# Kernel tuning notes

Hardware: AMD Instinct MI355X
Metric: run time of the kernel (lower is better)

Reference implementation:

```python
import jax, jax.numpy as jnp
import numpy as np

N_NODES = 100000
N_EDGES = 1600000
IN_C = 256
H1 = 128
H2 = 64
OUT_C = 64


def setup_inputs() -> dict:
    key = jax.random.key(0)
    ks = jax.random.split(key, 8)
    x = jax.random.normal(ks[0], (N_NODES, IN_C), dtype=jnp.float32)
    edge_src = jax.random.randint(ks[1], (N_EDGES,), 0, N_NODES, dtype=jnp.int32)
    edge_dst = jax.random.randint(ks[2], (N_EDGES,), 0, N_NODES, dtype=jnp.int32)
    edge_weight = jax.random.uniform(ks[3], (N_EDGES,), dtype=jnp.float32)
    W1 = jax.random.normal(ks[4], (IN_C, H1), dtype=jnp.float32) / np.sqrt(IN_C)
    b1 = jnp.zeros((H1,), dtype=jnp.float32)
    W2 = jax.random.normal(ks[5], (H1, H2), dtype=jnp.float32) / np.sqrt(H1)
    b2 = jnp.zeros((H2,), dtype=jnp.float32)
    W3 = jax.random.normal(ks[6], (H2, OUT_C), dtype=jnp.float32) / np.sqrt(H2)
    b3 = jnp.zeros((OUT_C,), dtype=jnp.float32)
    return dict(x=x, edge_src=edge_src, edge_dst=edge_dst, edge_weight=edge_weight,
                W1=W1, b1=b1, W2=W2, b2=b2, W3=W3, b3=b3)


def _gcn_layer(h, W, b, src, dst, ew):
    # GraphConvolution: out = adj @ (h @ W) + b, adj given as weighted edge list
    support = h @ W                      # [N, d_out] dense GEMM
    msg = support[src] * ew[:, None]     # [E, d_out] gather (irregular access)
    agg = jax.ops.segment_sum(msg, dst, num_segments=N_NODES)  # SpMM scatter-add
    return agg + b


def reference(x, edge_src, edge_dst, edge_weight, W1, b1, W2, b2, W3, b3):
    # Eval-mode forward: dropout is identity (training=False)
    h = jax.nn.relu(_gcn_layer(x, W1, b1, edge_src, edge_dst, edge_weight))
    h = jax.nn.relu(_gcn_layer(h, W2, b2, edge_src, edge_dst, edge_weight))
    out = _gcn_layer(h, W3, b3, edge_src, edge_dst, edge_weight)
    return out
```

## Files before the change

### kernel.cpp

```cpp
#include <hip/hip_runtime.h>
#include <hip/hip_bf16.h>


#define EPB 8192

__device__ __forceinline__ unsigned short f2bf(float f) {
    unsigned int u = __float_as_uint(f);
    unsigned int r = (u + 0x7fffu + ((u >> 16) & 1u)) >> 16;
    return (unsigned short)r;
}

using frag_ab = __attribute__((ext_vector_type(8))) short;
using frag_cd = __attribute__((ext_vector_type(4))) float;

template <int BN>
__global__ __launch_bounds__(256) void mfma_gemm_kernel(
    const float* __restrict__ A, const unsigned short* __restrict__ WT,
    unsigned short* __restrict__ C, int M, int K)
{
    constexpr int BM = 64, BK = 64;
    constexpr int LDA = BK + 8;
    __shared__ unsigned short As[BM * LDA];
    __shared__ unsigned short Bs[BN * LDA];

    const int tid = threadIdx.x;
    const int wave = tid >> 6;
    const int lane = tid & 63;
    const int quad = lane >> 4;
    const int l16 = lane & 15;
    const int m0 = blockIdx.x * BM;

    frag_cd acc[BN / 16];
#pragma unroll
    for (int f = 0; f < BN / 16; ++f) acc[f] = (frag_cd){0.f, 0.f, 0.f, 0.f};

    for (int k0 = 0; k0 < K; k0 += BK) {
#pragma unroll
        for (int i = 0; i < 4; ++i) {
            const int linear = (i * 256 + tid) * 4;
            const int r = linear >> 6;
            const int c = linear & 63;
            const int row = m0 + r;
            float4 v = make_float4(0.f, 0.f, 0.f, 0.f);
            if (row < M) v = *(const float4*)&A[(size_t)row * K + k0 + c];
            ushort4 u;
            u.x = f2bf(v.x); u.y = f2bf(v.y); u.z = f2bf(v.z); u.w = f2bf(v.w);
            *(ushort4*)&As[r * LDA + c] = u;
        }
#pragma unroll
        for (int i = 0; i < BN / 32; ++i) {
            const int linear = (i * 256 + tid) * 8;
            const int n = linear >> 6;
            const int c = linear & 63;
            const uint4 u = *(const uint4*)&WT[(size_t)n * K + k0 + c];
            *(uint4*)&Bs[n * LDA + c] = u;
        }
        __syncthreads();

#pragma unroll
        for (int ks = 0; ks < 2; ++ks) {
            const int kk = ks * 32 + quad * 8;
            const frag_ab a = *(const frag_ab*)&As[(wave * 16 + l16) * LDA + kk];
#pragma unroll
            for (int f = 0; f < BN / 16; ++f) {
                const frag_ab b = *(const frag_ab*)&Bs[(f * 16 + l16) * LDA + kk];
                acc[f] = __builtin_amdgcn_mfma_f32_16x16x32_bf16(a, b, acc[f], 0, 0, 0);
            }
        }
        __syncthreads();
    }

#pragma unroll
    for (int f = 0; f < BN / 16; ++f) {
#pragma unroll
        for (int r = 0; r < 4; ++r) {
            const int row = m0 + wave * 16 + quad * 4 + r;
            if (row < M) C[(size_t)row * BN + f * 16 + l16] = f2bf(acc[f][r]);
        }
    }
}

__global__ __launch_bounds__(256) void wt_kernel(
    const float* __restrict__ W1, const float* __restrict__ W2, const float* __restrict__ W3,
    unsigned short* __restrict__ WT1, unsigned short* __restrict__ WT2, unsigned short* __restrict__ WT3)
{
    const int i = blockIdx.x * 256 + threadIdx.x;
    const float* W; unsigned short* WT; int K, N, j;
    if (i < 32768)      { W = W1; WT = WT1; K = 256; N = 128; j = i; }
    else if (i < 40960) { W = W2; WT = WT2; K = 128; N = 64;  j = i - 32768; }
    else if (i < 45056) { W = W3; WT = WT3; K = 64;  N = 64;  j = i - 40960; }
    else return;
    const int n = j / K, k = j % K;
    WT[j] = f2bf(W[k * N + n]);
}

__global__ __launch_bounds__(256) void zero_int_kernel(int* __restrict__ p, int n)
{
    const int i = blockIdx.x * 256 + threadIdx.x;
    if (i < n) p[i] = 0;
}

__global__ __launch_bounds__(256) void hist_kernel(
    const int* __restrict__ dst, int* __restrict__ deg, int E)
{
    const int e = blockIdx.x * 256 + threadIdx.x;
    if (e < E) atomicAdd(&deg[dst[e]], 1);
}

__global__ __launch_bounds__(256) void scan1_kernel(
    const int* __restrict__ deg, int* __restrict__ offs, int* __restrict__ bsum, int n)
{
    __shared__ int tmp[256];
    const int i = blockIdx.x * 256 + threadIdx.x;
    const int v = (i < n) ? deg[i] : 0;
    tmp[threadIdx.x] = v;
    __syncthreads();
#pragma unroll
    for (int d = 1; d < 256; d <<= 1) {
        const int t = (threadIdx.x >= d) ? tmp[threadIdx.x - d] : 0;
        __syncthreads();
        tmp[threadIdx.x] += t;
        __syncthreads();
    }
    if (i < n) offs[i] = tmp[threadIdx.x] - v;
    if (threadIdx.x == 255) bsum[blockIdx.x] = tmp[255];
}

__global__ __launch_bounds__(512) void scan2_kernel(int* __restrict__ bsum, int nb)
{
    __shared__ int tmp[512];
    const int v = ((int)threadIdx.x < nb) ? bsum[threadIdx.x] : 0;
    tmp[threadIdx.x] = v;
    __syncthreads();
#pragma unroll
    for (int d = 1; d < 512; d <<= 1) {
        const int t = ((int)threadIdx.x >= d) ? tmp[threadIdx.x - d] : 0;
        __syncthreads();
        tmp[threadIdx.x] += t;
        __syncthreads();
    }
    if ((int)threadIdx.x < nb) bsum[threadIdx.x] = tmp[threadIdx.x] - v;
}

__global__ __launch_bounds__(256) void scan3_kernel(
    int* __restrict__ offs, const int* __restrict__ bsum, int n, int E)
{
    const int i = blockIdx.x * 256 + threadIdx.x;
    if (i < n) offs[i] += bsum[blockIdx.x];
    if (i == 0) offs[n] = E;
}

__global__ __launch_bounds__(256) void count_kernel(
    const int* __restrict__ dst, int* __restrict__ cmat, int E, int nblk, int nbuck)
{
    __shared__ int hist[1600];
    for (int i = threadIdx.x; i < nbuck; i += 256) hist[i] = 0;
    __syncthreads();
    const int base = blockIdx.x * EPB;
    const int end = min(base + EPB, E);
    for (int e = base + threadIdx.x; e < end; e += 256)
        atomicAdd(&hist[dst[e] >> 6], 1);
    __syncthreads();
    for (int i = threadIdx.x; i < nbuck; i += 256)
        cmat[(size_t)i * nblk + blockIdx.x] = hist[i];
}

__global__ __launch_bounds__(256) void scanA_kernel(
    int* __restrict__ data, int* __restrict__ psum, int L)
{
    __shared__ int tmp[256];
    const int b0 = blockIdx.x * 1024 + threadIdx.x * 4;
    int v[4] = {0, 0, 0, 0};
    if (b0 + 3 < L) { const int4 t = *(const int4*)&data[b0]; v[0]=t.x; v[1]=t.y; v[2]=t.z; v[3]=t.w; }
    else { for (int i = 0; i < 4; ++i) if (b0 + i < L) v[i] = data[b0 + i]; }
    const int s = v[0] + v[1] + v[2] + v[3];
    tmp[threadIdx.x] = s;
    __syncthreads();
#pragma unroll
    for (int d = 1; d < 256; d <<= 1) {
        const int t = (threadIdx.x >= d) ? tmp[threadIdx.x - d] : 0;
        __syncthreads();
        tmp[threadIdx.x] += t;
        __syncthreads();
    }
    int run = tmp[threadIdx.x] - s;
    int o[4];
#pragma unroll
    for (int i = 0; i < 4; ++i) { o[i] = run; run += v[i]; }
    if (b0 + 3 < L) { *(int4*)&data[b0] = make_int4(o[0], o[1], o[2], o[3]); }
    else { for (int i = 0; i < 4; ++i) if (b0 + i < L) data[b0 + i] = o[i]; }
    if (threadIdx.x == 255) psum[blockIdx.x] = tmp[255];
}

__global__ __launch_bounds__(1024) void scanB_kernel(int* __restrict__ psum, int nb)
{
    __shared__ int tmp[1024];
    const int v = ((int)threadIdx.x < nb) ? psum[threadIdx.x] : 0;
    tmp[threadIdx.x] = v;
    __syncthreads();
#pragma unroll
    for (int d = 1; d < 1024; d <<= 1) {
        const int t = ((int)threadIdx.x >= d) ? tmp[threadIdx.x - d] : 0;
        __syncthreads();
        tmp[threadIdx.x] += t;
        __syncthreads();
    }
    if ((int)threadIdx.x < nb) psum[threadIdx.x] = tmp[threadIdx.x] - v;
}

__global__ __launch_bounds__(256) void scanC_kernel(
    int* __restrict__ data, const int* __restrict__ psum, int L)
{
    const int i = blockIdx.x * 256 + threadIdx.x;
    if (i < L) data[i] += psum[i >> 10];
}

__global__ __launch_bounds__(256) void place_kernel(
    const int* __restrict__ src, const int* __restrict__ dst, const float* __restrict__ ew,
    const int* __restrict__ cmat, uint2* __restrict__ ebuck, int E, int nblk, int nbuck)
{
    __shared__ int cursor[1600];
    const int k = blockIdx.x;
    for (int i = threadIdx.x; i < nbuck; i += 256)
        cursor[i] = cmat[(size_t)i * nblk + k];
    __syncthreads();
    const int base = k * EPB;
    const int end = min(base + EPB, E);
    for (int e = base + threadIdx.x; e < end; e += 256) {
        const int d = dst[e];
        const int b = d >> 6;
        const int pos = atomicAdd(&cursor[b], 1);
        ebuck[pos] = make_uint2(((unsigned)src[e] << 6) | (unsigned)(d & 63),
                                __float_as_uint(ew[e]));
    }
}

__global__ __launch_bounds__(256) void sort2_kernel(
    const uint2* __restrict__ ebuck, const int* __restrict__ offs,
    uint2* __restrict__ ecsr, int N)
{
    __shared__ int cur[64];
    const int b = blockIdx.x;
    const int node0 = b << 6;
    const int nn = min(64, N - node0);
    if ((int)threadIdx.x < nn) cur[threadIdx.x] = offs[node0 + threadIdx.x];
    __syncthreads();
    const int j0 = offs[node0];
    const int j1 = offs[node0 + nn];
    for (int j = j0 + (int)threadIdx.x; j < j1; j += 256) {
        const uint2 ed = ebuck[j];
        const int dl = (int)(ed.x & 63u);
        const int pos = atomicAdd(&cur[dl], 1);
        ecsr[pos] = make_uint2(ed.x >> 6, ed.y);
    }
}

template <int D, int LOGT, bool RELU>
__global__ __launch_bounds__(256) void gather_agg_kernel(
    const unsigned short* __restrict__ S, const int* __restrict__ offs,
    const uint2* __restrict__ ecsr,
    const float* __restrict__ bias, float* __restrict__ out, int N)
{
    const int TPN = 1 << LOGT;
    const int gid = blockIdx.x * 256 + threadIdx.x;
    const int node = gid >> LOGT;
    if (node >= N) return;
    const int lane = gid & (TPN - 1);
    const int c8 = lane << 3;

    const int j0 = offs[node];
    const int j1 = offs[node + 1];

    float acc[8];
#pragma unroll
    for (int c = 0; c < 8; ++c) acc[c] = 0.f;

    for (int jb = j0; jb < j1; jb += TPN) {
        const int j = jb + lane;
        int myc = 0;
        float myw = 0.f;
        if (j < j1) {
            const uint2 p = ecsr[j];
            myc = (int)p.x;
            myw = __uint_as_float(p.y);
        }
        const int cnt = min(TPN, j1 - jb);
        for (int t = 0; t < cnt; ++t) {
            const int s = __shfl(myc, t, TPN);
            const float w = __shfl(myw, t, TPN);
            const uint4 v = *(const uint4*)&S[(size_t)s * D + c8];
#pragma unroll
            for (int q = 0; q < 4; ++q) {
                const unsigned int u = (&v.x)[q];
                const float lo = __uint_as_float(u << 16);
                const float hi = __uint_as_float(u & 0xffff0000u);
                acc[q * 2 + 0] += w * lo;
                acc[q * 2 + 1] += w * hi;
            }
        }
    }

#pragma unroll
    for (int c = 0; c < 8; ++c) {
        float v = acc[c] + bias[c8 + c];
        if (RELU) v = fmaxf(v, 0.f);
        acc[c] = v;
    }
    float4* op = (float4*)&out[(size_t)node * D + c8];
    op[0] = make_float4(acc[0], acc[1], acc[2], acc[3]);
    op[1] = make_float4(acc[4], acc[5], acc[6], acc[7]);
}

extern "C" void kernel_launch(void* const* d_in, const int* in_sizes, int n_in,
                              void* d_out, int out_size, void* d_ws, size_t ws_size,
                              hipStream_t stream)
{
    const float* x    = (const float*)d_in[0];
    const int*   esrc = (const int*)  d_in[1];
    const int*   edst = (const int*)  d_in[2];
    const float* ew   = (const float*)d_in[3];
    const float* W1   = (const float*)d_in[4];
    const float* b1   = (const float*)d_in[5];
    const float* W2   = (const float*)d_in[6];
    const float* b2   = (const float*)d_in[7];
    const float* W3   = (const float*)d_in[8];
    const float* b3   = (const float*)d_in[9];

    const int N = in_sizes[0] / 256;
    const int E = in_sizes[1];

    const int nbuck = (N + 63) >> 6;
    const int nblk = (E + EPB - 1) / EPB;
    const int L = nbuck * nblk;

    unsigned short* Sb = (unsigned short*)d_ws;
    float* H   = (float*)(Sb + (size_t)N * 128);
    unsigned short* WT1 = (unsigned short*)(H + (size_t)N * 128);
    unsigned short* WT2 = WT1 + 256 * 128;
    unsigned short* WT3 = WT2 + 128 * 64;
    uint2* ebuck = (uint2*)(WT3 + 64 * 64);
    uint2* ecsr  = ebuck + E;
    int* deg    = (int*)(ecsr + E);
    int* offs   = deg + N;
    int* bsum   = offs + N + 4;
    int* cmat   = bsum + 512;
    int* psum   = cmat + ((L + 3) & ~3);
    float* out  = (float*)d_out;

    const dim3 blk(256);
    const int nblkN = (N + 255) / 256;
    const int nblkE = (E + 255) / 256;
    const int mblocks = (N + 63) / 64;

    wt_kernel<<<(45056 + 255) / 256, blk, 0, stream>>>(W1, W2, W3, WT1, WT2, WT3);
    zero_int_kernel<<<nblkN, blk, 0, stream>>>(deg, N);
    hist_kernel<<<nblkE, blk, 0, stream>>>(edst, deg, E);
    scan1_kernel<<<nblkN, blk, 0, stream>>>(deg, offs, bsum, N);
    scan2_kernel<<<1, 512, 0, stream>>>(bsum, nblkN);
    scan3_kernel<<<nblkN, blk, 0, stream>>>(offs, bsum, N, E);
    count_kernel<<<nblk, blk, 0, stream>>>(edst, cmat, E, nblk, nbuck);
    scanA_kernel<<<(L + 1023) / 1024, blk, 0, stream>>>(cmat, psum, L);
    scanB_kernel<<<1, 1024, 0, stream>>>(psum, (L + 1023) / 1024);
    scanC_kernel<<<(L + 255) / 256, blk, 0, stream>>>(cmat, psum, L);
    place_kernel<<<nblk, blk, 0, stream>>>(esrc, edst, ew, cmat, ebuck, E, nblk, nbuck);
    sort2_kernel<<<nbuck, blk, 0, stream>>>(ebuck, offs, ecsr, N);

    mfma_gemm_kernel<128><<<mblocks, blk, 0, stream>>>(x, WT1, Sb, N, 256);
    gather_agg_kernel<128, 4, true><<<((N * 16) + 255) / 256, blk, 0, stream>>>(
        Sb, offs, ecsr, b1, H, N);

    mfma_gemm_kernel<64><<<mblocks, blk, 0, stream>>>(H, WT2, Sb, N, 128);
    gather_agg_kernel<64, 3, true><<<((N * 8) + 255) / 256, blk, 0, stream>>>(
        Sb, offs, ecsr, b2, H, N);

    mfma_gemm_kernel<64><<<mblocks, blk, 0, stream>>>(H, WT3, Sb, N, 64);
    gather_agg_kernel<64, 3, false><<<((N * 8) + 255) / 256, blk, 0, stream>>>(
        Sb, offs, ecsr, b3, out, N);
}
```

Measured before the change: 520.3 us.

## Derive CSR offsets in sort pass, enlarge GEMM row tile, unroll full gather chunks

The separate degree histogram and three-kernel scan are removed. Per-node CSR offsets are now computed inside sort2 from a local 64-bin count and wave prefix scan, with bucket bounds taken from the already-scanned count matrix. This drops five launches and a global atomic pass over all edges. The MFMA GEMM now computes 128 rows per block with two accumulator sets, so each B fragment is reused twice, at the cost of more registers and fewer blocks. The gather loop gains a fully unrolled fast path for full TPN chunks, with a masked tail loop for the remainder.

```diff
diff --git a/kernel.cpp b/kernel.cpp
--- a/kernel.cpp
+++ b/kernel.cpp
@@ -18,7 +18,7 @@
     const float* __restrict__ A, const unsigned short* __restrict__ WT,
     unsigned short* __restrict__ C, int M, int K)
 {
-    constexpr int BM = 64, BK = 64;
+    constexpr int BM = 128, BK = 64;
     constexpr int LDA = BK + 8;
     __shared__ unsigned short As[BM * LDA];
     __shared__ unsigned short Bs[BN * LDA];
@@ -30,13 +30,15 @@
     const int l16 = lane & 15;
     const int m0 = blockIdx.x * BM;
 
-    frag_cd acc[BN / 16];
-#pragma unroll
-    for (int f = 0; f < BN / 16; ++f) acc[f] = (frag_cd){0.f, 0.f, 0.f, 0.f};
+    frag_cd acc[2][BN / 16];
+#pragma unroll
+    for (int rt = 0; rt < 2; ++rt)
+#pragma unroll
+        for (int f = 0; f < BN / 16; ++f) acc[rt][f] = (frag_cd){0.f, 0.f, 0.f, 0.f};
 
     for (int k0 = 0; k0 < K; k0 += BK) {
 #pragma unroll
-        for (int i = 0; i < 4; ++i) {
+        for (int i = 0; i < 8; ++i) {
             const int linear = (i * 256 + tid) * 4;
             const int r = linear >> 6;
             const int c = linear & 63;
@@ -60,24 +62,27 @@
 #pragma unroll
         for (int ks = 0; ks < 2; ++ks) {
             const int kk = ks * 32 + quad * 8;
-            const frag_ab a = *(const frag_ab*)&As[(wave * 16 + l16) * LDA + kk];
+            const frag_ab a0 = *(const frag_ab*)&As[(wave * 32 + l16) * LDA + kk];
+            const frag_ab a1 = *(const frag_ab*)&As[(wave * 32 + 16 + l16) * LDA + kk];
 #pragma unroll
             for (int f = 0; f < BN / 16; ++f) {
                 const frag_ab b = *(const frag_ab*)&Bs[(f * 16 + l16) * LDA + kk];
-                acc[f] = __builtin_amdgcn_mfma_f32_16x16x32_bf16(a, b, acc[f], 0, 0, 0);
+                acc[0][f] = __builtin_amdgcn_mfma_f32_16x16x32_bf16(a0, b, acc[0][f], 0, 0, 0);
+                acc[1][f] = __builtin_amdgcn_mfma_f32_16x16x32_bf16(a1, b, acc[1][f], 0, 0, 0);
             }
         }
         __syncthreads();
     }
 
 #pragma unroll
-    for (int f = 0; f < BN / 16; ++f) {
-#pragma unroll
-        for (int r = 0; r < 4; ++r) {
-            const int row = m0 + wave * 16 + quad * 4 + r;
-            if (row < M) C[(size_t)row * BN + f * 16 + l16] = f2bf(acc[f][r]);
-        }
-    }
+    for (int rt = 0; rt < 2; ++rt)
+#pragma unroll
+        for (int f = 0; f < BN / 16; ++f)
+#pragma unroll
+            for (int r = 0; r < 4; ++r) {
+                const int row = m0 + wave * 32 + rt * 16 + quad * 4 + r;
+                if (row < M) C[(size_t)row * BN + f * 16 + l16] = f2bf(acc[rt][f][r]);
+            }
 }
 
 __global__ __launch_bounds__(256) void wt_kernel(
@@ -94,62 +99,6 @@
     WT[j] = f2bf(W[k * N + n]);
 }
 
-__global__ __launch_bounds__(256) void zero_int_kernel(int* __restrict__ p, int n)
-{
-    const int i = blockIdx.x * 256 + threadIdx.x;
-    if (i < n) p[i] = 0;
-}
-
-__global__ __launch_bounds__(256) void hist_kernel(
-    const int* __restrict__ dst, int* __restrict__ deg, int E)
-{
-    const int e = blockIdx.x * 256 + threadIdx.x;
-    if (e < E) atomicAdd(&deg[dst[e]], 1);
-}
-
-__global__ __launch_bounds__(256) void scan1_kernel(
-    const int* __restrict__ deg, int* __restrict__ offs, int* __restrict__ bsum, int n)
-{
-    __shared__ int tmp[256];
-    const int i = blockIdx.x * 256 + threadIdx.x;
-    const int v = (i < n) ? deg[i] : 0;
-    tmp[threadIdx.x] = v;
-    __syncthreads();
-#pragma unroll
-    for (int d = 1; d < 256; d <<= 1) {
-        const int t = (threadIdx.x >= d) ? tmp[threadIdx.x - d] : 0;
-        __syncthreads();
-        tmp[threadIdx.x] += t;
-        __syncthreads();
-    }
-    if (i < n) offs[i] = tmp[threadIdx.x] - v;
-    if (threadIdx.x == 255) bsum[blockIdx.x] = tmp[255];
-}
-
-__global__ __launch_bounds__(512) void scan2_kernel(int* __restrict__ bsum, int nb)
-{
-    __shared__ int tmp[512];
-    const int v = ((int)threadIdx.x < nb) ? bsum[threadIdx.x] : 0;
-    tmp[threadIdx.x] = v;
-    __syncthreads();
-#pragma unroll
-    for (int d = 1; d < 512; d <<= 1) {
-        const int t = ((int)threadIdx.x >= d) ? tmp[threadIdx.x - d] : 0;
-        __syncthreads();
-        tmp[threadIdx.x] += t;
-        __syncthreads();
-    }
-    if ((int)threadIdx.x < nb) bsum[threadIdx.x] = tmp[threadIdx.x] - v;
-}
-
-__global__ __launch_bounds__(256) void scan3_kernel(
-    int* __restrict__ offs, const int* __restrict__ bsum, int n, int E)
-{
-    const int i = blockIdx.x * 256 + threadIdx.x;
-    if (i < n) offs[i] += bsum[blockIdx.x];
-    if (i == 0) offs[n] = E;
-}
-
 __global__ __launch_bounds__(256) void count_kernel(
     const int* __restrict__ dst, int* __restrict__ cmat, int E, int nblk, int nbuck)
 {
@@ -236,21 +185,42 @@
 }
 
 __global__ __launch_bounds__(256) void sort2_kernel(
-    const uint2* __restrict__ ebuck, const int* __restrict__ offs,
-    uint2* __restrict__ ecsr, int N)
-{
+    const uint2* __restrict__ ebuck, const int* __restrict__ cmat,
+    int* __restrict__ offs, uint2* __restrict__ ecsr,
+    int N, int nblk, int nbuck, int E)
+{
+    __shared__ int cnt[64];
     __shared__ int cur[64];
     const int b = blockIdx.x;
     const int node0 = b << 6;
     const int nn = min(64, N - node0);
-    if ((int)threadIdx.x < nn) cur[threadIdx.x] = offs[node0 + threadIdx.x];
-    __syncthreads();
-    const int j0 = offs[node0];
-    const int j1 = offs[node0 + nn];
+    const int j0 = cmat[(size_t)b * nblk];
+    const int j1 = (b + 1 < nbuck) ? cmat[(size_t)(b + 1) * nblk] : E;
+
+    if (threadIdx.x < 64) cnt[threadIdx.x] = 0;
+    __syncthreads();
+    for (int j = j0 + (int)threadIdx.x; j < j1; j += 256)
+        atomicAdd(&cnt[ebuck[j].x & 63u], 1);
+    __syncthreads();
+
+    if (threadIdx.x < 64) {
+        const int myv = cnt[threadIdx.x];
+        int v = myv;
+#pragma unroll
+        for (int d = 1; d < 64; d <<= 1) {
+            const int t = __shfl_up(v, d, 64);
+            if ((int)threadIdx.x >= d) v += t;
+        }
+        const int base = j0 + v - myv;
+        cur[threadIdx.x] = base;
+        if ((int)threadIdx.x < nn) offs[node0 + threadIdx.x] = base;
+        if (threadIdx.x == 0 && b == nbuck - 1) offs[N] = E;
+    }
+    __syncthreads();
+
     for (int j = j0 + (int)threadIdx.x; j < j1; j += 256) {
         const uint2 ed = ebuck[j];
-        const int dl = (int)(ed.x & 63u);
-        const int pos = atomicAdd(&cur[dl], 1);
+        const int pos = atomicAdd(&cur[ed.x & 63u], 1);
         ecsr[pos] = make_uint2(ed.x >> 6, ed.y);
     }
 }
@@ -275,7 +245,25 @@
 #pragma unroll
     for (int c = 0; c < 8; ++c) acc[c] = 0.f;
 
-    for (int jb = j0; jb < j1; jb += TPN) {
+    int jb = j0;
+    for (; jb + TPN <= j1; jb += TPN) {
+        const uint2 p = ecsr[jb + lane];
+        const int myc = (int)p.x;
+        const float myw = __uint_as_float(p.y);
+#pragma unroll
+        for (int t = 0; t < TPN; ++t) {
+            const int s = __shfl(myc, t, TPN);
+            const float w = __shfl(myw, t, TPN);
+            const uint4 v = *(const uint4*)&S[(size_t)s * D + c8];
+#pragma unroll
+            for (int q = 0; q < 4; ++q) {
+                const unsigned int u = (&v.x)[q];
+                acc[q * 2 + 0] += w * __uint_as_float(u << 16);
+                acc[q * 2 + 1] += w * __uint_as_float(u & 0xffff0000u);
+            }
+        }
+    }
+    if (jb < j1) {
         const int j = jb + lane;
         int myc = 0;
         float myw = 0.f;
@@ -284,7 +272,7 @@
             myc = (int)p.x;
             myw = __uint_as_float(p.y);
         }
-        const int cnt = min(TPN, j1 - jb);
+        const int cnt = j1 - jb;
         for (int t = 0; t < cnt; ++t) {
             const int s = __shfl(myc, t, TPN);
             const float w = __shfl(myw, t, TPN);
@@ -292,10 +280,8 @@
 #pragma unroll
             for (int q = 0; q < 4; ++q) {
                 const unsigned int u = (&v.x)[q];
-                const float lo = __uint_as_float(u << 16);
-                const float hi = __uint_as_float(u & 0xffff0000u);
-                acc[q * 2 + 0] += w * lo;
-                acc[q * 2 + 1] += w * hi;
+                acc[q * 2 + 0] += w * __uint_as_float(u << 16);
+                acc[q * 2 + 1] += w * __uint_as_float(u & 0xffff0000u);
             }
         }
     }
@@ -340,30 +326,21 @@
     unsigned short* WT3 = WT2 + 128 * 64;
     uint2* ebuck = (uint2*)(WT3 + 64 * 64);
     uint2* ecsr  = ebuck + E;
-    int* deg    = (int*)(ecsr + E);
-    int* offs   = deg + N;
-    int* bsum   = offs + N + 4;
-    int* cmat   = bsum + 512;
+    int* offs   = (int*)(ecsr + E);
+    int* cmat   = offs + N + 4;
     int* psum   = cmat + ((L + 3) & ~3);
     float* out  = (float*)d_out;
 
     const dim3 blk(256);
-    const int nblkN = (N + 255) / 256;
-    const int nblkE = (E + 255) / 256;
-    const int mblocks = (N + 63) / 64;
+    const int mblocks = (N + 127) / 128;
 
     wt_kernel<<<(45056 + 255) / 256, blk, 0, stream>>>(W1, W2, W3, WT1, WT2, WT3);
-    zero_int_kernel<<<nblkN, blk, 0, stream>>>(deg, N);
-    hist_kernel<<<nblkE, blk, 0, stream>>>(edst, deg, E);
-    scan1_kernel<<<nblkN, blk, 0, stream>>>(deg, offs, bsum, N);
-    scan2_kernel<<<1, 512, 0, stream>>>(bsum, nblkN);
-    scan3_kernel<<<nblkN, blk, 0, stream>>>(offs, bsum, N, E);
     count_kernel<<<nblk, blk, 0, stream>>>(edst, cmat, E, nblk, nbuck);
     scanA_kernel<<<(L + 1023) / 1024, blk, 0, stream>>>(cmat, psum, L);
     scanB_kernel<<<1, 1024, 0, stream>>>(psum, (L + 1023) / 1024);
     scanC_kernel<<<(L + 255) / 256, blk, 0, stream>>>(cmat, psum, L);
     place_kernel<<<nblk, blk, 0, stream>>>(esrc, edst, ew, cmat, ebuck, E, nblk, nbuck);
-    sort2_kernel<<<nbuck, blk, 0, stream>>>(ebuck, offs, ecsr, N);
+    sort2_kernel<<<nbuck, blk, 0, stream>>>(ebuck, cmat, offs, ecsr, N, nblk, nbuck, E);
 
     mfma_gemm_kernel<128><<<mblocks, blk, 0, stream>>>(x, WT1, Sb, N, 256);
     gather_agg_kernel<128, 4, true><<<((N * 16) + 255) / 256, blk, 0, stream>>>(
```

New measurement: 465.0 us. -10.6%, faster.
